# Kernel tuning notes

Measured on AMD Instinct MI355X. Metric: run time of the kernel, lower is better.

Reference implementation:

```python
import jax, jax.numpy as jnp
import numpy as np

B, S, H = 2, 1024, 1024
NH, HD = 8, 128
E, TOPK, MI = 8, 2, 1024
SI = 2 * MI  # shared experts intermediate (n_shared_experts=2)
EPS = 1e-6
THETA = 10000.0


def setup_inputs() -> dict:
    key = jax.random.key(0)
    ks = jax.random.split(key, 16)
    w = lambda k, shp: (0.02 * jax.random.normal(k, shp, dtype=jnp.float32))
    # RoPE tables [S, HD]
    inv_freq = 1.0 / (THETA ** (np.arange(0, HD, 2, dtype=np.float32) / HD))
    t = np.arange(S, dtype=np.float32)
    freqs = np.outer(t, inv_freq)
    emb = np.concatenate([freqs, freqs], axis=-1)
    return {
        "hidden_states": jax.random.normal(ks[0], (B, S, H), dtype=jnp.float32),
        "ln1_w": jnp.ones((H,), jnp.float32),
        "ln2_w": jnp.ones((H,), jnp.float32),
        "q_w": w(ks[1], (H, H)),
        "k_w": w(ks[2], (H, H)),
        "v_w": w(ks[3], (H, H)),
        "o_w": w(ks[4], (H, H)),
        "cos": jnp.asarray(np.cos(emb), jnp.float32),
        "sin": jnp.asarray(np.sin(emb), jnp.float32),
        "gate_w": w(ks[5], (E, H)),
        "eg_w": w(ks[6], (E, MI, H)),
        "eu_w": w(ks[7], (E, MI, H)),
        "ed_w": w(ks[8], (E, H, MI)),
        "sg_w": w(ks[9], (SI, H)),
        "su_w": w(ks[10], (SI, H)),
        "sd_w": w(ks[11], (H, SI)),
    }


def _rmsnorm(x, w):
    return x * jax.lax.rsqrt(jnp.mean(x * x, axis=-1, keepdims=True) + EPS) * w


def _rotate_half(x):
    x1, x2 = jnp.split(x, 2, axis=-1)
    return jnp.concatenate([-x2, x1], axis=-1)


def _attention(x, q_w, k_w, v_w, o_w, cos, sin):
    b, s, h = x.shape
    q = (x @ q_w.T).reshape(b, s, NH, HD)
    k = (x @ k_w.T).reshape(b, s, NH, HD)
    v = (x @ v_w.T).reshape(b, s, NH, HD)
    c = cos[None, :s, None, :]
    sn = sin[None, :s, None, :]
    q = q * c + _rotate_half(q) * sn
    k = k * c + _rotate_half(k) * sn
    scores = jnp.einsum("bqhd,bkhd->bhqk", q, k) / jnp.sqrt(jnp.float32(HD))
    causal = jnp.tril(jnp.ones((s, s), dtype=bool))
    scores = jnp.where(causal[None, None], scores, -jnp.inf)
    p = jax.nn.softmax(scores, axis=-1)
    out = jnp.einsum("bhqk,bkhd->bqhd", p, v).reshape(b, s, h)
    return out @ o_w.T


def _mlp(x, gw, uw, dw):
    return (jax.nn.silu(x @ gw.T) * (x @ uw.T)) @ dw.T


def _moe(x, gate_w, eg_w, eu_w, ed_w, sg_w, su_w, sd_w):
    b, s, h = x.shape
    xt = x.reshape(-1, h)                              # [T, H]
    T = xt.shape[0]
    probs = jax.nn.softmax(xt @ gate_w.T, axis=-1)     # [T, E]
    rw, idx = jax.lax.top_k(probs, TOPK)               # [T, K]
    rw = rw / (jnp.sum(rw, axis=-1, keepdims=True) + 1e-20)  # norm_topk_prob
    # dense combine weights [T, E] (zero for unselected experts)
    w_full = jnp.zeros((T, E), xt.dtype).at[jnp.arange(T)[:, None], idx].add(rw)
    # dense all-expert compute, masked-combined (faithful to per-token loop math)
    g = jax.nn.silu(jnp.einsum("th,eih->tei", xt, eg_w))
    u = jnp.einsum("th,eih->tei", xt, eu_w)
    y = jnp.einsum("tei,ehi->teh", g * u, ed_w)        # [T, E, H]
    routed = jnp.einsum("teh,te->th", y, w_full)
    shared = _mlp(xt, sg_w, su_w, sd_w)
    return (routed + shared).reshape(b, s, h)


def reference(hidden_states, ln1_w, ln2_w, q_w, k_w, v_w, o_w, cos, sin,
              gate_w, eg_w, eu_w, ed_w, sg_w, su_w, sd_w):
    x = hidden_states
    x = x + _attention(_rmsnorm(x, ln1_w), q_w, k_w, v_w, o_w, cos, sin)
    x = x + _moe(_rmsnorm(x, ln2_w), gate_w, eg_w, eu_w, ed_w, sg_w, su_w, sd_w)
    return x
```

## Files before the change

### kernel.cpp

```cpp
#include <hip/hip_runtime.h>

#define B_   2
#define S_   1024
#define H_   1024
#define NH_  8
#define HD_  128
#define E_   8
#define MI_  1024
#define SI_  2048
#define T_   2048
#define CAP_ 2048

typedef unsigned short u16;
typedef __attribute__((ext_vector_type(4))) float f32x4;
typedef __attribute__((ext_vector_type(4))) unsigned short u16x4;
typedef __attribute__((ext_vector_type(8))) unsigned short u16x8;
typedef __attribute__((ext_vector_type(8))) __bf16 bf16x8;

__device__ __forceinline__ u16 f2bf(float f) {
  unsigned int u = __builtin_bit_cast(unsigned int, f);
  u = (u + 0x7fffu + ((u >> 16) & 1u)) >> 16;
  return (u16)u;
}
__device__ __forceinline__ float bf2f(u16 u) {
  return __builtin_bit_cast(float, (unsigned int)u << 16);
}
__device__ __forceinline__ float wave_sum(float v) {
#pragma unroll
  for (int o = 32; o; o >>= 1) v += __shfl_down(v, o, 64);
  return v;
}
__device__ __forceinline__ void gll16(const u16* g, u16* l) {
  __builtin_amdgcn_global_load_lds((const __attribute__((address_space(1))) void*)g,
                                   (__attribute__((address_space(3))) void*)l, 16, 0, 0);
}

__device__ __forceinline__ void cvt_moe_rows(
    int row0, int tid,
    const float* __restrict__ eg_w, const float* __restrict__ eu_w,
    const float* __restrict__ ed_w, const float* __restrict__ sg_w,
    const float* __restrict__ su_w, const float* __restrict__ sd_w,
    u16* __restrict__ egu, u16* __restrict__ edb,
    u16* __restrict__ sgu, u16* __restrict__ sdb) {
  const float* src[8];
  u16* dst[8];
#pragma unroll
  for (int g = 0; g < 8; g++) {
    int row = row0 + g;
    if (row < 20480) {
      int rel = row - 4096;
      int zu = rel >= 8192;
      int r = rel & 8191;
      int e = r >> 10, i = r & 1023;
      int orow = (i >> 4) * 32 + (i & 15) + (zu ? 16 : 0);
      src[g] = (zu ? eu_w : eg_w) + (long)r * 1024;
      dst[g] = egu + ((long)e * 2048 + orow) * 1024;
    } else if (row < 28672) {
      long f = (long)(row - 20480) * 1024;
      src[g] = ed_w + f;
      dst[g] = edb + f;
    } else if (row < 32768) {
      int rel = row - 28672;
      int zu = rel >= 2048;
      int i = rel & 2047;
      int orow = (i >> 4) * 32 + (i & 15) + (zu ? 16 : 0);
      src[g] = (zu ? su_w : sg_w) + (long)i * 1024;
      dst[g] = sgu + (long)orow * 1024;
    } else {
      long f = (long)(row - 32768) * 1024;
      src[g] = sd_w + f;
      dst[g] = sdb + f;
    }
  }
  f32x4 v[8];
#pragma unroll
  for (int g = 0; g < 8; g++)
    v[g] = __builtin_nontemporal_load((const f32x4*)src[g] + tid);
#pragma unroll
  for (int g = 0; g < 8; g++) {
    u16x4 o;
#pragma unroll
    for (int c = 0; c < 4; c++) o[c] = f2bf(v[g][c]);
    ((u16x4*)dst[g])[tid] = o;
  }
}

__global__ void cvt_all(const float* __restrict__ q_w, const float* __restrict__ k_w,
                        const float* __restrict__ v_w, const float* __restrict__ o_w,
                        u16* __restrict__ qwb,
                        const float* __restrict__ hidden, const float* __restrict__ ln1w,
                        u16* __restrict__ xn) {
  int bid = blockIdx.x, tid = threadIdx.x;
  if (bid >= 512) {
    int t = bid - 512;
    f32x4 v = ((const f32x4*)(hidden + (long)t * H_))[tid];
    float ss = v[0]*v[0] + v[1]*v[1] + v[2]*v[2] + v[3]*v[3];
    __shared__ float red[4];
    float s = wave_sum(ss);
    if ((tid & 63) == 0) red[tid >> 6] = s;
    __syncthreads();
    float r = rsqrtf((red[0] + red[1] + red[2] + red[3]) * (1.0f / H_) + 1e-6f);
    f32x4 wv = ((const f32x4*)ln1w)[tid];
    u16x4 o;
#pragma unroll
    for (int c = 0; c < 4; c++) o[c] = f2bf(v[c] * r * wv[c]);
    ((u16x4*)(xn + (long)t * H_))[tid] = o;
    return;
  }
  const float* src[8];
  u16* dst[8];
#pragma unroll
  for (int g = 0; g < 8; g++) {
    int row = bid * 8 + g;
    int seg = row >> 10;
    const float* in = (seg == 0) ? q_w : (seg == 1) ? k_w : (seg == 2) ? v_w : o_w;
    src[g] = in + (long)(row & 1023) * 1024;
    dst[g] = qwb + (long)row * 1024;
  }
  f32x4 v[8];
#pragma unroll
  for (int g = 0; g < 8; g++)
    v[g] = __builtin_nontemporal_load((const f32x4*)src[g] + tid);
#pragma unroll
  for (int g = 0; g < 8; g++) {
    u16x4 o;
#pragma unroll
    for (int c = 0; c < 4; c++) o[c] = f2bf(v[g][c]);
    ((u16x4*)dst[g])[tid] = o;
  }
}

__global__ void rmsnorm2_gate(const float* __restrict__ x1, const float* __restrict__ ln2w,
                              const float* __restrict__ gw, u16* __restrict__ xn,
                              int* __restrict__ eidx, float* __restrict__ aw) {
  int t = blockIdx.x, tid = threadIdx.x;
  int lane = tid & 63, wave = tid >> 6;
  f32x4 v = ((const f32x4*)(x1 + (long)t * H_))[tid];
  float ss = v[0]*v[0] + v[1]*v[1] + v[2]*v[2] + v[3]*v[3];
  __shared__ float redS[4];
  __shared__ float redE[4][E_];
  float s = wave_sum(ss);
  if (lane == 0) redS[wave] = s;
  __syncthreads();
  float r = rsqrtf((redS[0] + redS[1] + redS[2] + redS[3]) * (1.0f / H_) + 1e-6f);
  f32x4 wv = ((const f32x4*)ln2w)[tid];
  float xv[4];
  u16x4 o;
#pragma unroll
  for (int c = 0; c < 4; c++) { xv[c] = v[c] * r * wv[c]; o[c] = f2bf(xv[c]); }
  ((u16x4*)(xn + (long)t * H_))[tid] = o;
  float acc[E_];
#pragma unroll
  for (int e = 0; e < E_; e++) {
    f32x4 g = ((const f32x4*)(gw + (long)e * H_))[tid];
    acc[e] = xv[0]*g[0] + xv[1]*g[1] + xv[2]*g[2] + xv[3]*g[3];
  }
#pragma unroll
  for (int e = 0; e < E_; e++) acc[e] = wave_sum(acc[e]);
  if (lane == 0)
#pragma unroll
    for (int e = 0; e < E_; e++) redE[wave][e] = acc[e];
  __syncthreads();
  if (tid == 0) {
    float l[E_];
#pragma unroll
    for (int e = 0; e < E_; e++) l[e] = redE[0][e] + redE[1][e] + redE[2][e] + redE[3][e];
    float mx = l[0];
#pragma unroll
    for (int e = 1; e < E_; e++) mx = fmaxf(mx, l[e]);
    float p[E_], z = 0.f;
#pragma unroll
    for (int e = 0; e < E_; e++) { p[e] = __expf(l[e] - mx); z += p[e]; }
    int e0 = 0;
#pragma unroll
    for (int e = 1; e < E_; e++) if (p[e] > p[e0]) e0 = e;
    int e1 = (e0 == 0) ? 1 : 0;
#pragma unroll
    for (int e = 0; e < E_; e++) if (e != e0 && p[e] > p[e1]) e1 = e;
    float q0 = p[e0] / z, q1 = p[e1] / z;
    float invs = 1.0f / (q0 + q1 + 1e-20f);
    eidx[t * 2] = e0;
    eidx[t * 2 + 1] = e1;
    aw[t * 2] = q0 * invs;
    aw[t * 2 + 1] = q1 * invs;
  }
}

__global__ __launch_bounds__(256) void route_scan(const int* __restrict__ eidx,
                                                  int* __restrict__ arow,
                                                  int* __restrict__ cursor,
                                                  int* __restrict__ itok,
                                                  int* __restrict__ wlist) {
  __shared__ int sc[E_][256];
  int tid = threadIdx.x;
  unsigned c0 = 0, c1 = 0;
  int ebuf[16];
#pragma unroll
  for (int i = 0; i < 16; i++) {
    int e = eidx[tid * 16 + i];
    ebuf[i] = e;
    if (e < 4) c0 += 1u << (8 * e); else c1 += 1u << (8 * (e - 4));
  }
#pragma unroll
  for (int e = 0; e < E_; e++)
    sc[e][tid] = (e < 4) ? (int)((c0 >> (8 * e)) & 0xff) : (int)((c1 >> (8 * (e - 4))) & 0xff);
  __syncthreads();
  for (int st = 1; st < 256; st <<= 1) {
    int v[E_];
#pragma unroll
    for (int e = 0; e < E_; e++) v[e] = (tid >= st) ? sc[e][tid - st] : 0;
    __syncthreads();
#pragma unroll
    for (int e = 0; e < E_; e++) sc[e][tid] += v[e];
    __syncthreads();
  }
  if (tid == 255) {
    int w = 0;
#pragma unroll
    for (int e = 0; e < E_; e++) {
      int cnt = sc[e][255];
      cursor[e] = cnt;
      int nt = (min(cnt, CAP_) + 127) >> 7;
      for (int mt = 0; mt < nt; mt++) wlist[w++] = (e << 8) | mt;
    }
    for (int mt = 0; mt < 16; mt++) wlist[w++] = (1 << 16) | mt;
    for (; w < 56; w++) wlist[w] = -1;
  }
  int base[E_];
#pragma unroll
  for (int e = 0; e < E_; e++) {
    int own = (e < 4) ? (int)((c0 >> (8 * e)) & 0xff) : (int)((c1 >> (8 * (e - 4))) & 0xff);
    base[e] = sc[e][tid] - own;
  }
  __syncthreads();
#pragma unroll
  for (int e = 0; e < E_; e++) sc[e][tid] = base[e];
  __syncthreads();
  unsigned r0 = 0, r1 = 0;
#pragma unroll
  for (int i = 0; i < 16; i++) {
    int e = ebuf[i];
    int run = (e < 4) ? (int)((r0 >> (8 * e)) & 0xff) : (int)((r1 >> (8 * (e - 4))) & 0xff);
    int row = e * CAP_ + sc[e][tid] + run;
    arow[tid * 16 + i] = row;
    itok[row] = (tid * 16 + i) >> 1;
    if (e < 4) r0 += 1u << (8 * e); else r1 += 1u << (8 * (e - 4));
  }
}

__global__ void rope_vtrans(const u16* __restrict__ qkvb, const float* __restrict__ cs,
                            const float* __restrict__ sn, u16* __restrict__ qb,
                            u16* __restrict__ kb, u16* __restrict__ vt) {
  int bid = blockIdx.x, tid = threadIdx.x;
  if (bid < 1024) {
    int z = bid >> 9;
    const u16* src = qkvb + (long)z * 2097152;
    u16* dstb = z ? kb : qb;
    int rb = (bid & 511) * 32 + (tid >> 3);
    int u = tid & 7;
    int h = rb & 7, bs = rb >> 3, s = bs & 1023, b = bs >> 10;
    const u16* row = src + (long)rb * 128;
    int d0 = u * 8;
    u16x8 v1 = *(const u16x8*)(row + d0);
    u16x8 v2 = *(const u16x8*)(row + d0 + 64);
    const float* c1 = cs + s * 128 + d0;
    const float* s1 = sn + s * 128 + d0;
    u16x8 o1, o2;
#pragma unroll
    for (int c = 0; c < 8; c++) {
      float a = bf2f(v1[c]), q2 = bf2f(v2[c]);
      o1[c] = f2bf(a * c1[c] - q2 * s1[c]);
      o2[c] = f2bf(q2 * c1[c + 64] + a * s1[c + 64]);
    }
    u16* orow = dstb + ((long)((b * NH_ + h) * S_ + s)) * HD_;
    *(u16x8*)(orow + d0) = o1;
    *(u16x8*)(orow + d0 + 64) = o2;
  } else {
    int vb = bid - 1024;
    int bh = vb >> 5;
    int rem = vb & 31;
    int s0 = (rem >> 1) * 64, d0 = (rem & 1) * 64;
    int b = bh >> 3, h = bh & 7;
    __shared__ u16 tile[64][68];
    const u16* vsrc = qkvb + 2 * 2097152;
#pragma unroll
    for (int it = 0; it < 4; it++) {
      int idx = it * 256 + tid;
      int r = idx >> 4, c = (idx & 15) * 4;
      u16x4 vv = *(const u16x4*)(vsrc + (((long)(b * S_ + s0 + r)) * NH_ + h) * HD_ + d0 + c);
      *(u16x4*)&tile[r][c] = vv;
    }
    __syncthreads();
#pragma unroll
    for (int it = 0; it < 4; it++) {
      int idx = it * 256 + tid;
      int dr = idx >> 4, sc = (idx & 15) * 4;
      u16x4 ov;
#pragma unroll
      for (int k = 0; k < 4; k++) ov[k] = tile[sc + k][dr];
      *(u16x4*)(vt + ((long)bh * HD_ + d0 + dr) * S_ + s0 + sc) = ov;
    }
  }
}

__global__ __launch_bounds__(256) void flash_cvt(
    const u16* __restrict__ qb, const u16* __restrict__ kb,
    const u16* __restrict__ vt, u16* __restrict__ Po,
    float* __restrict__ Pm, float* __restrict__ Pl,
    const float* __restrict__ eg_w, const float* __restrict__ eu_w,
    const float* __restrict__ ed_w, const float* __restrict__ sg_w,
    const float* __restrict__ su_w, const float* __restrict__ sd_w,
    u16* __restrict__ egu, u16* __restrict__ edb,
    u16* __restrict__ sgu, u16* __restrict__ sdb) {
  int bid = blockIdx.x;
  int tid = threadIdx.x;
  if (bid >= 640) {
    int row0 = 4096 + (bid - 640) * 8;
    cvt_moe_rows(row0, tid, eg_w, eu_w, ed_w, sg_w, su_w, sd_w, egu, edb, sgu, sdb);
    return;
  }
  int item = bid % 40;
  int bh = bid / 40;
  int qt, ch;
  if (item < 4)       { qt = item;                    ch = 0; }
  else if (item < 12) { qt = 4 + ((item - 4) >> 1);   ch = (item - 4) & 1; }
  else if (item < 24) { qt = 8 + (item - 12) / 3;     ch = (item - 12) % 3; }
  else                { qt = 12 + ((item - 24) >> 2); ch = (item - 24) & 3; }
  int j0 = ch * 4, j1 = min(j0 + 4, qt + 1);

  int wavei = tid >> 6, lane = tid & 63;
  int la = lane & 15, qd = lane >> 4;

  __shared__ __align__(16) u16 Ks[64 * 128];
  __shared__ __align__(16) u16 Vs[128 * 64];
  __shared__ __align__(16) u16 Ps[4][16 * 64];

  bf16x8 qf[4];
  const u16* qrow = qb + ((long)bh * S_ + qt * 64 + wavei * 16 + la) * HD_;
#pragma unroll
  for (int ks = 0; ks < 4; ks++)
    qf[ks] = *(const bf16x8*)(qrow + ks * 32 + qd * 8);

  f32x4 oacc[8];
#pragma unroll
  for (int nf = 0; nf < 8; nf++) oacc[nf] = (f32x4){0.f, 0.f, 0.f, 0.f};
  float m_i[4], l_i[4];
#pragma unroll
  for (int r = 0; r < 4; r++) { m_i[r] = -1e30f; l_i[r] = 0.f; }

  const u16* Kbase = kb + (long)bh * S_ * HD_;
  const u16* Vbase = vt + (long)bh * HD_ * S_;
  const float scale = 0.08838834764831845f;
  u16* pw = (u16*)Ps[wavei];
  int swz = la & 7;

  for (int j = j0; j < j1; j++) {
    __syncthreads();
#pragma unroll
    for (int t = 0; t < 4; t++) {
      int blk = t * 4 + wavei;
      int kr = blk * 4 + (lane >> 4);
      int kc = (lane & 15) ^ (kr & 7);
      gll16(Kbase + ((long)j * 64 + kr) * 128 + kc * 8, Ks + blk * 512);
      int vr = blk * 8 + (lane >> 3);
      int vc = (lane & 7) ^ (vr & 7);
      gll16(Vbase + (long)vr * 1024 + j * 64 + vc * 8, Vs + blk * 512);
    }
    __syncthreads();

    f32x4 sacc[4];
#pragma unroll
    for (int jf = 0; jf < 4; jf++) sacc[jf] = (f32x4){0.f, 0.f, 0.f, 0.f};
#pragma unroll
    for (int ks = 0; ks < 4; ks++)
#pragma unroll
      for (int jf = 0; jf < 4; jf++) {
        bf16x8 kfrag = *(const bf16x8*)(Ks + (jf * 16 + la) * 128 + ((ks * 4 + qd) ^ swz) * 8);
        sacc[jf] = __builtin_amdgcn_mfma_f32_16x16x32_bf16(qf[ks], kfrag, sacc[jf], 0, 0, 0);
      }

    float sv[4][4];
    int qglob = qt * 64 + wavei * 16 + qd * 4;
#pragma unroll
    for (int jf = 0; jf < 4; jf++) {
      int kglob = j * 64 + jf * 16 + la;
#pragma unroll
      for (int r = 0; r < 4; r++)
        sv[jf][r] = (kglob <= qglob + r) ? sacc[jf][r] * scale : -1e30f;
    }
    float mnew[4], alpha[4];
#pragma unroll
    for (int r = 0; r < 4; r++) {
      float mx = fmaxf(fmaxf(sv[0][r], sv[1][r]), fmaxf(sv[2][r], sv[3][r]));
#pragma unroll
      for (int o = 1; o < 16; o <<= 1) mx = fmaxf(mx, __shfl_xor(mx, o, 64));
      mnew[r] = fmaxf(m_i[r], mx);
      alpha[r] = __expf(m_i[r] - mnew[r]);
      m_i[r] = mnew[r];
    }
#pragma unroll
    for (int r = 0; r < 4; r++) {
      float sum = 0.f;
#pragma unroll
      for (int jf = 0; jf < 4; jf++) {
        float p = __expf(sv[jf][r] - mnew[r]);
        sv[jf][r] = p;
        sum += p;
      }
#pragma unroll
      for (int o = 1; o < 16; o <<= 1) sum += __shfl_xor(sum, o, 64);
      l_i[r] = l_i[r] * alpha[r] + sum;
    }
#pragma unroll
    for (int jf = 0; jf < 4; jf++)
#pragma unroll
      for (int r = 0; r < 4; r++) {
        int rp = qd * 4 + r;
        int e = jf * 16 + la;
        pw[rp * 64 + (((e >> 3) ^ (rp & 7)) << 3) + (e & 7)] = f2bf(sv[jf][r]);
      }
#pragma unroll
    for (int nf = 0; nf < 8; nf++)
#pragma unroll
      for (int r = 0; r < 4; r++) oacc[nf][r] *= alpha[r];
#pragma unroll
    for (int ks = 0; ks < 2; ks++) {
      bf16x8 pfrag = *(const bf16x8*)(pw + la * 64 + ((ks * 4 + qd) ^ swz) * 8);
#pragma unroll
      for (int nf = 0; nf < 8; nf++) {
        bf16x8 vfrag = *(const bf16x8*)(Vs + (nf * 16 + la) * 64 + (((ks * 4 + qd) & 7) ^ swz) * 8);
        oacc[nf] = __builtin_amdgcn_mfma_f32_16x16x32_bf16(pfrag, vfrag, oacc[nf], 0, 0, 0);
      }
    }
  }

  int pidx = (bh * 16 + qt) * 4 + ch;
  int rowb = wavei * 16 + qd * 4;
  u16* pob = Po + ((long)pidx * 64 + rowb) * 128;
#pragma unroll
  for (int r = 0; r < 4; r++)
#pragma unroll
    for (int nf = 0; nf < 8; nf++)
      pob[(long)r * 128 + nf * 16 + la] = f2bf(oacc[nf][r]);
  if (la == 0)
#pragma unroll
    for (int r = 0; r < 4; r++) {
      Pm[pidx * 64 + rowb + r] = m_i[r];
      Pl[pidx * 64 + rowb + r] = l_i[r];
    }
}

__global__ __launch_bounds__(256) void attn_merge(
    const u16* __restrict__ Po, const float* __restrict__ Pm,
    const float* __restrict__ Pl, u16* __restrict__ attn) {
  int qt = blockIdx.x, bh = blockIdx.y;
  int b = bh >> 3, h = bh & 7;
  int nch = (qt >> 2) + 1;
  int t = threadIdx.x;
  int row = t >> 2, cg = (t & 3) * 32;
  long base = (long)(bh * 16 + qt) * 4;
  float mv[4], wv[4];
  float M = -1e30f;
  for (int c = 0; c < nch; c++) { mv[c] = Pm[(base + c) * 64 + row]; M = fmaxf(M, mv[c]); }
  float L = 0.f;
  for (int c = 0; c < nch; c++) { wv[c] = __expf(mv[c] - M); L += wv[c] * Pl[(base + c) * 64 + row]; }
  float inv = 1.0f / L;
  f32x4 o[8];
#pragma unroll
  for (int k = 0; k < 8; k++) o[k] = (f32x4){0.f, 0.f, 0.f, 0.f};
  for (int c = 0; c < nch; c++) {
    const u16x4* src = (const u16x4*)(Po + ((base + c) * 64 + row) * 128 + cg);
#pragma unroll
    for (int k = 0; k < 8; k++) {
      u16x4 sv = src[k];
#pragma unroll
      for (int e = 0; e < 4; e++) o[k][e] += bf2f(sv[e]) * wv[c];
    }
  }
  u16* dst = attn + ((long)b * S_ + qt * 64 + row) * H_ + h * HD_ + cg;
#pragma unroll
  for (int k = 0; k < 8; k++) {
    u16x4 ov;
#pragma unroll
    for (int c = 0; c < 4; c++) ov[c] = f2bf(o[k][c] * inv);
    ((u16x4*)dst)[k] = ov;
  }
}

__global__ void final_combine(const float* __restrict__ x1, const float* __restrict__ ys,
                              const u16* __restrict__ y, const int* __restrict__ arow,
                              const float* __restrict__ aw, float* __restrict__ out) {
  int t = blockIdx.x;
  int i = threadIdx.x * 4;
  int r0 = arow[t * 2], r1 = arow[t * 2 + 1];
  float w0 = aw[t * 2], w1 = aw[t * 2 + 1];
  f32x4 a = *(const f32x4*)(x1 + (long)t * H_ + i);
  f32x4 b = *(const f32x4*)(ys + (long)t * H_ + i);
  u16x4 y0 = *(const u16x4*)(y + (long)r0 * H_ + i);
  u16x4 y1 = *(const u16x4*)(y + (long)r1 * H_ + i);
  f32x4 o;
#pragma unroll
  for (int c = 0; c < 4; c++)
    o[c] = a[c] + b[c] + w0 * bf2f(y0[c]) + w1 * bf2f(y1[c]);
  *(f32x4*)(out + (long)t * H_ + i) = o;
}

template <int MT, int STORE_BF16, int ADD_RES, int FUSE_SILU, int IND, int WL>
__global__ __launch_bounds__(256) void gemm_bt(
    const u16* __restrict__ Ag, const u16* __restrict__ Bg, void* __restrict__ Cg,
    const float* __restrict__ Res, int K, int lda, int ldb, int ldc,
    long sAz, long sBz, long sCz, const int* __restrict__ mlimit,
    const int* __restrict__ itok, const int* __restrict__ wlist,
    const u16* __restrict__ Ag2, const u16* __restrict__ Bg2, void* __restrict__ Cg2,
    int lda2, int ldb2, int ldc2, int K2, int nx0, int nx1) {
  constexpr int MR = MT / 32;
  int z = 0, m0, kind = 0;
  const u16 *A, *B;
  void* C;
  long cbase;
  bool ind = (IND != 0);
  if constexpr (WL == 2) {
    int wv = wlist[blockIdx.y];
    if (wv < 0) return;
    kind = wv >> 16;
    if ((int)blockIdx.x >= (kind ? nx1 : nx0)) return;
    m0 = (wv & 255) * MT;
    if (kind) {
      A = Ag2; B = Bg2; C = Cg2;
      lda = lda2; ldb = ldb2; ldc = ldc2; K = K2;
      ind = false;
      cbase = 0;
    } else {
      z = (wv >> 8) & 255;
      A = Ag + (IND ? 0 : z * sAz);
      B = Bg + z * sBz;
      C = Cg;
      cbase = (long)z * sCz;
    }
  } else {
    z = blockIdx.z;
    m0 = blockIdx.y * MT;
    if (mlimit && m0 >= mlimit[z]) return;
    A = Ag + (IND ? 0 : z * sAz);
    B = Bg + z * sBz;
    C = Cg;
    cbase = (long)z * sCz;
  }
  int n0 = blockIdx.x * 128;

  __shared__ __align__(16) u16 As[2][MT * 64];
  __shared__ __align__(16) u16 Bs[2][128 * 64];
  int tid = threadIdx.x;
  int lane = tid & 63, wave = tid >> 6;
  int wm = (wave & 1) * (MT / 2), wn = (wave >> 1) * 64;
  int la = lane & 15, qd = lane >> 4;
  int sr = lane >> 3;
  int scs = (lane & 7) ^ (sr & 7);

  const u16* ap[MT / 32];
  const u16* bp[4];
#pragma unroll
  for (int t = 0; t < MT / 32; t++) {
    int rloc = m0 + t * 32 + wave * 8 + sr;
    long arow_g = (IND && ind) ? (long)itok[(long)z * CAP_ + rloc] : (long)rloc;
    ap[t] = A + arow_g * lda + scs * 8;
  }
#pragma unroll
  for (int t = 0; t < 4; t++)
    bp[t] = B + (long)(n0 + t * 32 + wave * 8 + sr) * ldb + scs * 8;

  f32x4 acc[MR][4];
#pragma unroll
  for (int i = 0; i < MR; i++)
#pragma unroll
    for (int j = 0; j < 4; j++) acc[i][j] = (f32x4){0.f, 0.f, 0.f, 0.f};

  auto stage = [&](int buf, int k0) {
#pragma unroll
    for (int t = 0; t < MT / 32; t++)
      gll16(ap[t] + k0, &As[buf][(t * 32 + wave * 8) * 64]);
#pragma unroll
    for (int t = 0; t < 4; t++)
      gll16(bp[t] + k0, &Bs[buf][(t * 32 + wave * 8) * 64]);
  };

  int sw = la & 7;
  int nt = K >> 6;
  int cur = 0;
  stage(0, 0);
  for (int t = 0; t < nt; ++t) {
    if (t + 1 < nt) {
      stage(cur ^ 1, (t + 1) * 64);
      if constexpr (MT == 128)
        asm volatile("s_waitcnt vmcnt(8)" ::: "memory");
      else
        asm volatile("s_waitcnt vmcnt(6)" ::: "memory");
    } else {
      asm volatile("s_waitcnt vmcnt(0)" ::: "memory");
    }
    __builtin_amdgcn_s_barrier();
#pragma unroll
    for (int kk = 0; kk < 2; kk++) {
      bf16x8 af[MR], bfv[4];
#pragma unroll
      for (int i = 0; i < MR; i++)
        af[i] = *(const bf16x8*)(&As[cur][0] + (wm + i * 16 + la) * 64 + (((kk * 4 + qd) ^ sw) << 3));
#pragma unroll
      for (int j = 0; j < 4; j++)
        bfv[j] = *(const bf16x8*)(&Bs[cur][0] + (wn + j * 16 + la) * 64 + (((kk * 4 + qd) ^ sw) << 3));
#pragma unroll
      for (int i = 0; i < MR; i++)
#pragma unroll
        for (int j = 0; j < 4; j++)
          acc[i][j] = __builtin_amdgcn_mfma_f32_16x16x32_bf16(af[i], bfv[j], acc[i][j], 0, 0, 0);
    }
    __builtin_amdgcn_s_barrier();
    cur ^= 1;
  }

  if (FUSE_SILU) {
#pragma unroll
    for (int i = 0; i < MR; i++) {
#pragma unroll
      for (int jp = 0; jp < 2; jp++) {
        int hcol = ((n0 + wn) >> 1) + (jp << 4) + la;
#pragma unroll
        for (int r = 0; r < 4; r++) {
          int row = m0 + wm + i * 16 + qd * 4 + r;
          float g = acc[i][jp * 2][r], u = acc[i][jp * 2 + 1][r];
          float sg = g / (1.f + __expf(-g));
          ((u16*)C)[cbase + (long)row * ldc + hcol] = f2bf(sg * u);
        }
      }
    }
  } else {
    bool sbf = (WL == 2) ? (kind == 0) : (STORE_BF16 != 0);
#pragma unroll
    for (int i = 0; i < MR; i++) {
#pragma unroll
      for (int j = 0; j < 4; j++) {
        int col = n0 + wn + j * 16 + la;
#pragma unroll
        for (int r = 0; r < 4; r++) {
          int row = m0 + wm + i * 16 + qd * 4 + r;
          float v = acc[i][j][r];
          long ci = cbase + (long)row * ldc + col;
          if (ADD_RES) v += Res[(long)row * ldc + col];
          if (sbf) ((u16*)C)[ci] = f2bf(v);
          else ((float*)C)[ci] = v;
        }
      }
    }
  }
}

extern "C" void kernel_launch(void* const* d_in, const int* in_sizes, int n_in,
                              void* d_out, int out_size, void* d_ws, size_t ws_size,
                              hipStream_t stream) {
  const float* hidden = (const float*)d_in[0];
  const float* ln1w = (const float*)d_in[1];
  const float* ln2w = (const float*)d_in[2];
  const float* q_w = (const float*)d_in[3];
  const float* k_w = (const float*)d_in[4];
  const float* v_w = (const float*)d_in[5];
  const float* o_w = (const float*)d_in[6];
  const float* cosp = (const float*)d_in[7];
  const float* sinp = (const float*)d_in[8];
  const float* gate_w = (const float*)d_in[9];
  const float* eg_w = (const float*)d_in[10];
  const float* eu_w = (const float*)d_in[11];
  const float* ed_w = (const float*)d_in[12];
  const float* sg_w = (const float*)d_in[13];
  const float* su_w = (const float*)d_in[14];
  const float* sd_w = (const float*)d_in[15];
  float* out = (float*)d_out;

  char* w = (char*)d_ws;
  const size_t MB = 1u << 20;
  u16* qwb = (u16*)(w + 0 * MB);
  u16* egu = (u16*)(w + 8 * MB);
  u16* edb = (u16*)(w + 40 * MB);
  u16* sgu = (u16*)(w + 56 * MB);
  u16* sdb = (u16*)(w + 64 * MB);
  float* x1 = (float*)(w + 68 * MB);
  u16* xn = (u16*)(w + 76 * MB);
  u16* attn = (u16*)(w + 80 * MB);
  int* cursor = (int*)(w + 84 * MB);
  int* arow = (int*)(w + 84 * MB + 1024);
  float* aw = (float*)(w + 84 * MB + 20 * 1024);
  int* eidx = (int*)(w + 84 * MB + 40 * 1024);
  int* itok = (int*)(w + 84 * MB + 60 * 1024);
  int* wlist = (int*)(w + 84 * MB + 128 * 1024);
  u16* qkvb = (u16*)(w + 85 * MB);
  u16* qb = (u16*)(w + 109 * MB);
  u16* kb = (u16*)(w + 113 * MB);
  u16* vt = (u16*)(w + 117 * MB);
  u16* Po = (u16*)(w + 121 * MB);
  float* Pm = (float*)(w + 155 * MB);
  float* Pl = (float*)(w + 156 * MB);
  u16* hbuf = (u16*)(w + 121 * MB);
  u16* y = (u16*)(w + 157 * MB);
  u16* hs = (u16*)(w + 189 * MB);
  float* ys = (float*)(w + 197 * MB);

  const long M1 = 1048576, M2 = 2097152;

  cvt_all<<<2560, 256, 0, stream>>>(q_w, k_w, v_w, o_w, qwb, hidden, ln1w, xn);

  gemm_bt<128, 1, 0, 0, 0, 0><<<dim3(8, 16, 3), 256, 0, stream>>>(
      xn, qwb, qkvb, nullptr, 1024, 1024, 1024, 1024, 0, M1, M2, nullptr, nullptr,
      nullptr, nullptr, nullptr, nullptr, 0, 0, 0, 0, 0, 0);
  rope_vtrans<<<1536, 256, 0, stream>>>(qkvb, cosp, sinp, qb, kb, vt);
  flash_cvt<<<640 + 3840, 256, 0, stream>>>(qb, kb, vt, Po, Pm, Pl,
                                            eg_w, eu_w, ed_w, sg_w, su_w, sd_w,
                                            egu, edb, sgu, sdb);
  attn_merge<<<dim3(16, 16), 256, 0, stream>>>(Po, Pm, Pl, attn);
  gemm_bt<64, 0, 1, 0, 0, 0><<<dim3(8, 32, 1), 256, 0, stream>>>(
      attn, qwb + 3 * M1, x1, hidden, 1024, 1024, 1024, 1024, 0, 0, 0, nullptr, nullptr,
      nullptr, nullptr, nullptr, nullptr, 0, 0, 0, 0, 0, 0);

  rmsnorm2_gate<<<T_, 256, 0, stream>>>(x1, ln2w, gate_w, xn, eidx, aw);
  hipMemsetAsync(itok, 0, E_ * CAP_ * 4, stream);
  route_scan<<<1, 256, 0, stream>>>(eidx, arow, cursor, itok, wlist);
  gemm_bt<128, 1, 0, 1, 1, 2><<<dim3(32, 56, 1), 256, 0, stream>>>(
      xn, egu, hbuf, nullptr, 1024, 1024, 1024, MI_,
      0, (long)2 * MI_ * H_, (long)CAP_ * MI_, nullptr, itok, wlist,
      xn, sgu, hs, 1024, 1024, SI_, 1024, 16, 32);
  gemm_bt<128, 1, 0, 0, 0, 2><<<dim3(8, 56, 1), 256, 0, stream>>>(
      hbuf, edb, y, nullptr, 1024, 1024, 1024, 1024,
      (long)CAP_ * MI_, (long)H_ * MI_, (long)CAP_ * H_, nullptr, nullptr, wlist,
      hs, sdb, ys, 2048, 2048, 1024, 2048, 8, 8);

  final_combine<<<T_, 256, 0, stream>>>(x1, ys, y, arow, aw, out);
}
```

Measured before the change: 383.0 us.

## Use 256x256-tile GEMM kernel for fused gate/up MoE projection

Adds a dedicated 512-thread kernel with 256x256 output tiles, double-buffered LDS staging and a fused SiLU*up epilogue for the routed-expert and shared-expert gate/up GEMM. The route scan now also emits a 256-row work list for it. Larger tiles raise arithmetic intensity and cut redundant global loads of the weights and gathered activations. The cost is 128KB of LDS per block, heavy register use limiting occupancy, and more padded work on partially filled expert tiles.

Result: no change. 380.6 us (-0.6%).

```diff
diff --git a/kernel.cpp b/kernel.cpp
--- a/kernel.cpp
+++ b/kernel.cpp
@@ -190,7 +190,8 @@
                                                   int* __restrict__ arow,
                                                   int* __restrict__ cursor,
                                                   int* __restrict__ itok,
-                                                  int* __restrict__ wlist) {
+                                                  int* __restrict__ wlist,
+                                                  int* __restrict__ wl256) {
   __shared__ int sc[E_][256];
   int tid = threadIdx.x;
   unsigned c0 = 0, c1 = 0;
@@ -215,16 +216,21 @@
     __syncthreads();
   }
   if (tid == 255) {
-    int w = 0;
+    int w = 0, w2 = 0;
 #pragma unroll
     for (int e = 0; e < E_; e++) {
       int cnt = sc[e][255];
       cursor[e] = cnt;
-      int nt = (min(cnt, CAP_) + 127) >> 7;
+      int cc = min(cnt, CAP_);
+      int nt = (cc + 127) >> 7;
       for (int mt = 0; mt < nt; mt++) wlist[w++] = (e << 8) | mt;
+      int nt2 = (cc + 255) >> 8;
+      for (int mt = 0; mt < nt2; mt++) wl256[w2++] = (e << 8) | mt;
     }
     for (int mt = 0; mt < 16; mt++) wlist[w++] = (1 << 16) | mt;
     for (; w < 56; w++) wlist[w] = -1;
+    for (int mt = 0; mt < 8; mt++) wl256[w2++] = (1 << 16) | mt;
+    for (; w2 < 32; w2++) wl256[w2] = -1;
   }
   int base[E_];
 #pragma unroll
@@ -503,6 +509,108 @@
   for (int c = 0; c < 4; c++)
     o[c] = a[c] + b[c] + w0 * bf2f(y0[c]) + w1 * bf2f(y1[c]);
   *(f32x4*)(out + (long)t * H_ + i) = o;
+}
+
+__global__ __launch_bounds__(512) void gemm256(
+    const u16* __restrict__ Ag, const u16* __restrict__ Bg, u16* __restrict__ Cg,
+    int K, int lda, int ldb, int ldc, long sBz, long sCz,
+    const int* __restrict__ itok, const int* __restrict__ wl256,
+    const u16* __restrict__ Bg2, u16* __restrict__ Cg2,
+    int ldb2, int ldc2, int nx0, int nx1) {
+  int wv = wl256[blockIdx.y];
+  if (wv < 0) return;
+  int kind = wv >> 16;
+  if ((int)blockIdx.x >= (kind ? nx1 : nx0)) return;
+  int m0 = (wv & 255) << 8;
+  int z = (wv >> 8) & 255;
+  const u16 *A = Ag, *B;
+  u16* C;
+  long cbase;
+  bool ind;
+  if (kind) { B = Bg2; C = Cg2; ldb = ldb2; ldc = ldc2; cbase = 0; ind = false; }
+  else      { B = Bg + (long)z * sBz; C = Cg; cbase = (long)z * sCz; ind = true; }
+  int n0 = blockIdx.x * 256;
+
+  __shared__ __align__(16) u16 As[2][256 * 64];
+  __shared__ __align__(16) u16 Bs[2][256 * 64];
+  int tid = threadIdx.x;
+  int lane = tid & 63, wave = tid >> 6;
+  int wr = wave >> 2, wc = wave & 3;
+  int wm = wr * 128, wn = wc * 64;
+  int la = lane & 15, qd = lane >> 4;
+  int sr = lane >> 3;
+  int scs = (lane & 7) ^ (sr & 7);
+
+  const u16* ap[4];
+  const u16* bp[4];
+#pragma unroll
+  for (int r = 0; r < 4; r++) {
+    int rloc = m0 + r * 64 + wave * 8 + sr;
+    long arow_g = ind ? (long)itok[(long)z * CAP_ + rloc] : (long)rloc;
+    ap[r] = A + arow_g * lda + scs * 8;
+    bp[r] = B + (long)(n0 + r * 64 + wave * 8 + sr) * ldb + scs * 8;
+  }
+
+  f32x4 acc[8][4];
+#pragma unroll
+  for (int i = 0; i < 8; i++)
+#pragma unroll
+    for (int j = 0; j < 4; j++) acc[i][j] = (f32x4){0.f, 0.f, 0.f, 0.f};
+
+  auto stage = [&](int buf, int k0) {
+#pragma unroll
+    for (int r = 0; r < 4; r++)
+      gll16(ap[r] + k0, &As[buf][(r * 64 + wave * 8) * 64]);
+#pragma unroll
+    for (int r = 0; r < 4; r++)
+      gll16(bp[r] + k0, &Bs[buf][(r * 64 + wave * 8) * 64]);
+  };
+
+  int sw = la & 7;
+  int nt = K >> 6;
+  int cur = 0;
+  stage(0, 0);
+  for (int t = 0; t < nt; ++t) {
+    if (t + 1 < nt) {
+      stage(cur ^ 1, (t + 1) * 64);
+      asm volatile("s_waitcnt vmcnt(8)" ::: "memory");
+    } else {
+      asm volatile("s_waitcnt vmcnt(0)" ::: "memory");
+    }
+    __builtin_amdgcn_s_barrier();
+#pragma unroll
+    for (int kk = 0; kk < 2; kk++) {
+      bf16x8 af[8], bfv[4];
+#pragma unroll
+      for (int i = 0; i < 8; i++)
+        af[i] = *(const bf16x8*)(&As[cur][0] + (wm + i * 16 + la) * 64 + (((kk * 4 + qd) ^ sw) << 3));
+#pragma unroll
+      for (int j = 0; j < 4; j++)
+        bfv[j] = *(const bf16x8*)(&Bs[cur][0] + (wn + j * 16 + la) * 64 + (((kk * 4 + qd) ^ sw) << 3));
+#pragma unroll
+      for (int i = 0; i < 8; i++)
+#pragma unroll
+        for (int j = 0; j < 4; j++)
+          acc[i][j] = __builtin_amdgcn_mfma_f32_16x16x32_bf16(af[i], bfv[j], acc[i][j], 0, 0, 0);
+    }
+    __builtin_amdgcn_s_barrier();
+    cur ^= 1;
+  }
+
+#pragma unroll
+  for (int i = 0; i < 8; i++) {
+#pragma unroll
+    for (int jp = 0; jp < 2; jp++) {
+      int hcol = ((n0 + wn) >> 1) + (jp << 4) + la;
+#pragma unroll
+      for (int r = 0; r < 4; r++) {
+        int row = m0 + wm + i * 16 + qd * 4 + r;
+        float g = acc[i][jp * 2][r], u = acc[i][jp * 2 + 1][r];
+        float sg = g / (1.f + __expf(-g));
+        C[cbase + (long)row * ldc + hcol] = f2bf(sg * u);
+      }
+    }
+  }
 }
 
 template <int MT, int STORE_BF16, int ADD_RES, int FUSE_SILU, int IND, int WL>
@@ -691,6 +799,7 @@
   int* eidx = (int*)(w + 84 * MB + 40 * 1024);
   int* itok = (int*)(w + 84 * MB + 60 * 1024);
   int* wlist = (int*)(w + 84 * MB + 128 * 1024);
+  int* wl256 = (int*)(w + 84 * MB + 132 * 1024);
   u16* qkvb = (u16*)(w + 85 * MB);
   u16* qb = (u16*)(w + 109 * MB);
   u16* kb = (u16*)(w + 113 * MB);
@@ -721,11 +830,11 @@
 
   rmsnorm2_gate<<<T_, 256, 0, stream>>>(x1, ln2w, gate_w, xn, eidx, aw);
   hipMemsetAsync(itok, 0, E_ * CAP_ * 4, stream);
-  route_scan<<<1, 256, 0, stream>>>(eidx, arow, cursor, itok, wlist);
-  gemm_bt<128, 1, 0, 1, 1, 2><<<dim3(32, 56, 1), 256, 0, stream>>>(
-      xn, egu, hbuf, nullptr, 1024, 1024, 1024, MI_,
-      0, (long)2 * MI_ * H_, (long)CAP_ * MI_, nullptr, itok, wlist,
-      xn, sgu, hs, 1024, 1024, SI_, 1024, 16, 32);
+  route_scan<<<1, 256, 0, stream>>>(eidx, arow, cursor, itok, wlist, wl256);
+  gemm256<<<dim3(16, 32, 1), 512, 0, stream>>>(
+      xn, egu, hbuf, 1024, 1024, 1024, MI_,
+      (long)2 * MI_ * H_, (long)CAP_ * MI_, itok, wl256,
+      sgu, hs, 1024, SI_, 8, 16);
   gemm_bt<128, 1, 0, 0, 0, 2><<<dim3(8, 56, 1), 256, 0, stream>>>(
       hbuf, edb, y, nullptr, 1024, 1024, 1024, 1024,
       (long)CAP_ * MI_, (long)H_ * MI_, (long)CAP_ * H_, nullptr, nullptr, wlist,
```
